# Kernel tuning notes

Measured on AMD Instinct MI355X. Metric: run time of the kernel, lower is better.

## Reference

```python
import jax, jax.numpy as jnp
import numpy as np

EPS = 1e-7
N = 100000
E = 1600000
IN_DIM = 128
OUT_DIM = 128


def _norm(t):
    # clamped L2 norm over last dim, keepdims
    return jnp.clip(jnp.linalg.norm(t, axis=-1, keepdims=True), EPS, None)


def log_map_zero(x, c):
    sqrt_c = jnp.sqrt(c)
    xn = _norm(x)
    y = jnp.clip(sqrt_c * xn, None, 1.0 - 1e-5)
    return jnp.arctanh(y) * x / (sqrt_c * xn)


def exp_map_zero(v, c):
    sqrt_c = jnp.sqrt(c)
    vn = _norm(v)
    return jnp.tanh(sqrt_c * vn) * v / (sqrt_c * vn)


def setup_inputs() -> dict:
    key = jax.random.key(0)
    k1, k2, k3, k4 = jax.random.split(key, 4)
    x = 0.1 * jax.random.normal(k1, (N, IN_DIM), dtype=jnp.float32)  # inside ball
    edge_index = jax.random.randint(k2, (2, E), 0, N, dtype=jnp.int64)
    c = jnp.ones((), dtype=jnp.float32)
    # Xavier-uniform weight (out_dim, in_dim)
    limit = float(np.sqrt(6.0 / (IN_DIM + OUT_DIM)))
    weight = jax.random.uniform(k3, (OUT_DIM, IN_DIM), minval=-limit, maxval=limit, dtype=jnp.float32)
    bias = jnp.zeros((OUT_DIM,), dtype=jnp.float32)
    return {"x": x, "edge_index": edge_index, "c": c, "num_nodes": N,
            "weight": weight, "bias": bias}


def reference(x, edge_index, c, num_nodes, weight, bias):
    # 1. log-map all node features to tangent space at origin
    v = log_map_zero(x, c)  # (N, in_dim)
    src, dst = edge_index[0], edge_index[1]
    # 2. mean aggregation over neighbours (incl. self) via segment_sum
    agg = jax.ops.segment_sum(v[src], dst, num_segments=num_nodes) + v
    count = jax.ops.segment_sum(jnp.ones((src.shape[0],), dtype=v.dtype), dst,
                                num_segments=num_nodes) + 1.0
    v_agg = agg / jnp.clip(count, 1.0, None)[:, None]
    # 3. back to hyperbolic space, then hyperbolic linear
    x_hyp = exp_map_zero(v_agg, c)
    v2 = log_map_zero(x_hyp, c)
    out = v2 @ weight.T + bias
    return exp_map_zero(out, c)
```

## Files before the change

### kernel.cpp

```cpp
#include <hip/hip_runtime.h>
#include <math.h>

#define EPSF 1e-7f
#define YMAXF 0.99999f
#define WPITCH 136

#define NBUCK 256
#define PB_CHUNK 2048

typedef short bf16x8 __attribute__((ext_vector_type(8)));
typedef short bf16x4 __attribute__((ext_vector_type(4)));
typedef float f32x4  __attribute__((ext_vector_type(4)));
typedef int   i32x4  __attribute__((ext_vector_type(4)));

__device__ __forceinline__ float grp32_sum(float v) {
    v += __shfl_xor(v, 1);
    v += __shfl_xor(v, 2);
    v += __shfl_xor(v, 4);
    v += __shfl_xor(v, 8);
    v += __shfl_xor(v, 16);
    return v;
}

__device__ __forceinline__ short f2bf(float f) {
    unsigned u = __float_as_uint(f);
    unsigned r = (u + 0x7FFFu + ((u >> 16) & 1u)) >> 16;
    return (short)r;
}

__device__ __forceinline__ float bf2f(short u) {
    return __uint_as_float(((unsigned)(unsigned short)u) << 16);
}

__device__ __forceinline__ float bf_lo(int w) {
    return __uint_as_float(((unsigned)w) << 16);
}
__device__ __forceinline__ float bf_hi(int w) {
    return __uint_as_float(((unsigned)w) & 0xffff0000u);
}

__global__ void logmap_kernel(const float* __restrict__ x,
                              const float* __restrict__ c_ptr,
                              short* __restrict__ v_bf,
                              int N) {
    int gid = blockIdx.x * blockDim.x + threadIdx.x;
    int row = gid >> 5;
    if (row >= N) return;
    int lane = gid & 31;
    const float4 xv = ((const float4*)x)[(size_t)row * 32 + lane];
    float ss = xv.x * xv.x + xv.y * xv.y + xv.z * xv.z + xv.w * xv.w;
    ss = grp32_sum(ss);
    float sc = sqrtf(c_ptr[0]);
    float xn = fmaxf(sqrtf(ss), EPSF);
    float y = fminf(sc * xn, YMAXF);
    float s = atanhf(y) / (sc * xn);
    bf16x4 pk;
    pk[0] = f2bf(s * xv.x); pk[1] = f2bf(s * xv.y);
    pk[2] = f2bf(s * xv.z); pk[3] = f2bf(s * xv.w);
    *(bf16x4*)&v_bf[(size_t)row * 128 + lane * 4] = pk;
}

__global__ __launch_bounds__(256)
void bucket_count_kernel(const int* __restrict__ eidx_dst,
                         int* __restrict__ bucketCount, int E) {
    __shared__ int h[NBUCK];
    int tid = threadIdx.x;
    h[tid] = 0;
    __syncthreads();
    int per = (E + gridDim.x - 1) / gridDim.x;
    int start = blockIdx.x * per;
    int end = min(start + per, E);
    for (int i = start + tid; i < end; i += 256)
        atomicAdd(&h[eidx_dst[i] >> 9], 1);
    __syncthreads();
    if (h[tid]) atomicAdd(&bucketCount[tid], h[tid]);
}

__global__ __launch_bounds__(256)
void bucket_scan_kernel(const int* __restrict__ bucketCount,
                        int* __restrict__ bucket_base,
                        int* __restrict__ cursor) {
    __shared__ int part[256];
    int tid = threadIdx.x;
    int val = bucketCount[tid];
    part[tid] = val;
    __syncthreads();
    for (int off = 1; off < 256; off <<= 1) {
        int t = (tid >= off) ? part[tid - off] : 0;
        __syncthreads();
        part[tid] += t;
        __syncthreads();
    }
    int excl = part[tid] - val;
    bucket_base[tid] = excl;
    cursor[tid] = excl;
}

__global__ __launch_bounds__(256)
void bucket_scatter_kernel(const int* __restrict__ eidx,
                           int* __restrict__ cursor,
                           int* __restrict__ bucketed, int E) {
    __shared__ int hist[NBUCK];
    __shared__ int lstart[NBUCK];
    __shared__ int gbase[NBUCK];
    __shared__ int part[256];
    __shared__ int stage[PB_CHUNK];
    __shared__ unsigned char stageB[PB_CHUNK];

    int tid = threadIdx.x;
    int start = blockIdx.x * PB_CHUNK;
    int cnt = min(PB_CHUNK, E - start);
    hist[tid] = 0;
    __syncthreads();

    const int J = PB_CHUNK / 256;
    int myP[J], myB[J], myR[J];
    #pragma unroll
    for (int j = 0; j < J; ++j) {
        int idx = j * 256 + tid;
        myR[j] = -1;
        if (idx < cnt) {
            int e = start + idx;
            int d = eidx[E + e];
            int s = eidx[e];
            int b = d >> 9;
            myB[j] = b;
            myP[j] = ((d & 511) << 17) | s;
            myR[j] = atomicAdd(&hist[b], 1);
        }
    }
    __syncthreads();
    part[tid] = hist[tid];
    __syncthreads();
    for (int off = 1; off < 256; off <<= 1) {
        int t = (tid >= off) ? part[tid - off] : 0;
        __syncthreads();
        part[tid] += t;
        __syncthreads();
    }
    lstart[tid] = part[tid] - hist[tid];
    if (hist[tid]) gbase[tid] = atomicAdd(&cursor[tid], hist[tid]);
    __syncthreads();
    #pragma unroll
    for (int j = 0; j < J; ++j) {
        if (myR[j] >= 0) {
            int pos = lstart[myB[j]] + myR[j];
            stage[pos] = myP[j];
            stageB[pos] = (unsigned char)myB[j];
        }
    }
    __syncthreads();
    for (int i = tid; i < cnt; i += 256) {
        int b = stageB[i];
        bucketed[gbase[b] + (i - lstart[b])] = stage[i];
    }
}

__global__ __launch_bounds__(256)
void csr_kernel(const int* __restrict__ bucketed,
                const int* __restrict__ bucket_base,
                const int* __restrict__ cursor_post,
                int* __restrict__ offsets, int* __restrict__ deg,
                int* __restrict__ sorted_src, int N) {
    __shared__ int hist[512];
    __shared__ int pre[512];
    __shared__ int cur[512];
    __shared__ int part[256];
    int b = blockIdx.x;
    int tid = threadIdx.x;
    int start = bucket_base[b];
    int end = cursor_post[b];
    hist[tid] = 0;
    hist[tid + 256] = 0;
    __syncthreads();
    for (int i = start + tid; i < end; i += 256)
        atomicAdd(&hist[bucketed[i] >> 17], 1);
    __syncthreads();
    int a0 = hist[2 * tid], a1 = hist[2 * tid + 1];
    part[tid] = a0 + a1;
    __syncthreads();
    for (int off = 1; off < 256; off <<= 1) {
        int t = (tid >= off) ? part[tid - off] : 0;
        __syncthreads();
        part[tid] += t;
        __syncthreads();
    }
    int base2 = part[tid] - (a0 + a1);
    pre[2 * tid] = base2;
    pre[2 * tid + 1] = base2 + a0;
    cur[2 * tid] = base2;
    cur[2 * tid + 1] = base2 + a0;
    __syncthreads();
    int node0 = b << 9;
    for (int i = tid; i < 512; i += 256) {
        int node = node0 + i;
        if (node < N) { offsets[node] = start + pre[i]; deg[node] = hist[i]; }
    }
    for (int i = start + tid; i < end; i += 256) {
        int p = bucketed[i];
        int ld = p >> 17;
        int src = p & 0x1FFFF;
        int r = atomicAdd(&cur[ld], 1);
        sorted_src[start + r] = src;
    }
}

__global__ __launch_bounds__(256, 3)
void gather_epilogue_kernel(const short* __restrict__ v_bf,
                            const int* __restrict__ sorted_src,
                            const int* __restrict__ offsets,
                            const int* __restrict__ deg,
                            const float* __restrict__ W,
                            const float* __restrict__ bias,
                            const float* __restrict__ c_ptr,
                            float* __restrict__ out,
                            int N) {
    __shared__ short Wl[128 * WPITCH];
    __shared__ short v2l[64 * WPITCH];

    int tid = threadIdx.x;
    for (int i = tid; i < 4096; i += 256) {
        float4 w4 = ((const float4*)W)[i];
        int o = i >> 5;
        int k = (i & 31) * 4;
        bf16x4 w;
        w[0] = f2bf(w4.x); w[1] = f2bf(w4.y); w[2] = f2bf(w4.z); w[3] = f2bf(w4.w);
        *(bf16x4*)&Wl[o * WPITCH + k] = w;
    }

    int wave = tid >> 6;
    int lane = tid & 63;
    int quad = lane >> 4;
    int l16  = lane & 15;
    int g  = tid >> 4;
    int gl = tid & 15;
    float sc = sqrtf(c_ptr[0]);

    float bsv[8];
    #pragma unroll
    for (int c = 0; c < 8; ++c) bsv[c] = bias[c * 16 + l16];

    int row_base = blockIdx.x * 64;

    for (int t = 0; t < 4; ++t) {
        int row = row_base + t * 16 + g;
        bool valid = (row < N);
        float acc[8];
        #pragma unroll
        for (int i = 0; i < 8; ++i) acc[i] = 0.0f;
        int start = 0, d = 0;
        if (valid) {
            start = offsets[row];
            d = deg[row];
            bf16x8 r0 = *(const bf16x8*)&v_bf[(size_t)row * 128 + gl * 8];
            i32x4 w0 = *(const i32x4*)&r0;
            #pragma unroll
            for (int k2 = 0; k2 < 4; ++k2) {
                acc[2 * k2]     = bf_lo(w0[k2]);
                acc[2 * k2 + 1] = bf_hi(w0[k2]);
            }
        }
        for (int j = 0; j < d; j += 16) {
            int m = d - j;
            int batch = sorted_src[start + min(j + gl, d - 1)];

            bf16x8 q0, q1, q2, q3, q4, q5, q6, q7,
                   q8, q9, qA, qB, qC, qD, qE, qF;
#define GLD(i, dst) do {                                                      \
        int src_ = __shfl(batch, (lane & 48) | (i));                          \
        unsigned voff_ = ((unsigned)src_ << 8) | (unsigned)(gl << 4);         \
        asm volatile("global_load_dwordx4 %0, %1, %2"                         \
                     : "=v"(dst) : "v"(voff_), "s"(v_bf));                    \
    } while (0)
            GLD(0, q0);  GLD(1, q1);  GLD(2, q2);  GLD(3, q3);
            GLD(4, q4);  GLD(5, q5);  GLD(6, q6);  GLD(7, q7);
            GLD(8, q8);  GLD(9, q9);  GLD(10, qA); GLD(11, qB);
            GLD(12, qC); GLD(13, qD); GLD(14, qE); GLD(15, qF);
#undef GLD
            asm volatile("s_waitcnt vmcnt(0)" ::: "memory");
            __builtin_amdgcn_sched_barrier(0);

#define ACC(i, rsrc) do {                                                     \
        float w_ = ((i) < m) ? 1.0f : 0.0f;                                   \
        i32x4 wv_ = *(i32x4*)&(rsrc);                                         \
        acc[0] = fmaf(bf_lo(wv_[0]), w_, acc[0]);                             \
        acc[1] = fmaf(bf_hi(wv_[0]), w_, acc[1]);                             \
        acc[2] = fmaf(bf_lo(wv_[1]), w_, acc[2]);                             \
        acc[3] = fmaf(bf_hi(wv_[1]), w_, acc[3]);                             \
        acc[4] = fmaf(bf_lo(wv_[2]), w_, acc[4]);                             \
        acc[5] = fmaf(bf_hi(wv_[2]), w_, acc[5]);                             \
        acc[6] = fmaf(bf_lo(wv_[3]), w_, acc[6]);                             \
        acc[7] = fmaf(bf_hi(wv_[3]), w_, acc[7]);                             \
    } while (0)
            ACC(0, q0);  ACC(1, q1);  ACC(2, q2);  ACC(3, q3);
            ACC(4, q4);  ACC(5, q5);  ACC(6, q6);  ACC(7, q7);
            ACC(8, q8);  ACC(9, q9);  ACC(10, qA); ACC(11, qB);
            ACC(12, qC); ACC(13, qD); ACC(14, qE); ACC(15, qF);
#undef ACC
        }
        float inv = 1.0f / (float)(d + 1);
        #pragma unroll
        for (int i = 0; i < 8; ++i) acc[i] *= inv;

        float ss = 0.0f;
        #pragma unroll
        for (int i = 0; i < 8; ++i) ss += acc[i] * acc[i];
        ss += __shfl_xor(ss, 1);
        ss += __shfl_xor(ss, 2);
        ss += __shfl_xor(ss, 4);
        ss += __shfl_xor(ss, 8);

        float vn  = sqrtf(ss);
        float vnc = fmaxf(vn, EPSF);
        float th  = tanhf(sc * vnc);
        float tt  = th / (sc * vnc);
        float hn  = fmaxf(th / sc, EPSF);
        float y2  = fminf(sc * hn, YMAXF);
        float s2  = atanhf(y2) / (sc * hn);
        float scale = s2 * tt;

        bf16x8 pk;
        #pragma unroll
        for (int i = 0; i < 8; ++i) pk[i] = f2bf(acc[i] * scale);
        *(bf16x8*)&v2l[(t * 16 + g) * WPITCH + gl * 8] = pk;
    }
    __syncthreads();

    f32x4 acc2[8];
    #pragma unroll
    for (int c = 0; c < 8; ++c) acc2[c] = (f32x4){bsv[c], bsv[c], bsv[c], bsv[c]};
    #pragma unroll
    for (int k0 = 0; k0 < 128; k0 += 32) {
        bf16x8 af = *(const bf16x8*)&v2l[(wave * 16 + l16) * WPITCH + k0 + quad * 8];
        #pragma unroll
        for (int c = 0; c < 8; ++c) {
            bf16x8 bf = *(const bf16x8*)&Wl[(c * 16 + l16) * WPITCH + k0 + quad * 8];
            acc2[c] = __builtin_amdgcn_mfma_f32_16x16x32_bf16(af, bf, acc2[c], 0, 0, 0);
        }
    }

    #pragma unroll
    for (int r = 0; r < 4; ++r) {
        float ss = 0.0f;
        #pragma unroll
        for (int c = 0; c < 8; ++c) ss += acc2[c][r] * acc2[c][r];
        ss += __shfl_xor(ss, 1);
        ss += __shfl_xor(ss, 2);
        ss += __shfl_xor(ss, 4);
        ss += __shfl_xor(ss, 8);
        float on  = sqrtf(ss);
        float onc = fmaxf(on, EPSF);
        float gsc = tanhf(sc * onc) / (sc * onc);
        int orow = row_base + wave * 16 + quad * 4 + r;
        if (orow < N) {
            size_t base = (size_t)orow * 128;
            #pragma unroll
            for (int c = 0; c < 8; ++c)
                out[base + c * 16 + l16] = gsc * acc2[c][r];
        }
    }
}

extern "C" void kernel_launch(void* const* d_in, const int* in_sizes, int n_in,
                              void* d_out, int out_size, void* d_ws, size_t ws_size,
                              hipStream_t stream) {
    const float* x     = (const float*)d_in[0];
    const int*   eidx  = (const int*)d_in[1];
    const float* c_ptr = (const float*)d_in[2];
    const float* W     = (const float*)d_in[4];
    const float* bias  = (const float*)d_in[5];
    float* out = (float*)d_out;

    int N = in_sizes[0] / 128;
    int E = in_sizes[1] / 2;

    short* v_bf        = (short*)d_ws;
    int*   deg         = (int*)(v_bf + (size_t)N * 128);
    int*   offsets     = deg + N;
    int*   bucketCount = offsets + N;
    int*   bucket_base = bucketCount + NBUCK;
    int*   cursor      = bucket_base + NBUCK;
    int*   bucketed    = cursor + NBUCK;
    int*   sorted_src  = bucketed + E;

    hipMemsetAsync(bucketCount, 0, NBUCK * sizeof(int), stream);

    {
        long long threads = (long long)N * 32;
        int blocks = (int)((threads + 255) / 256);
        hipLaunchKernelGGL(logmap_kernel, dim3(blocks), dim3(256), 0, stream,
                           x, c_ptr, v_bf, N);
    }
    hipLaunchKernelGGL(bucket_count_kernel, dim3(256), dim3(256), 0, stream,
                       eidx + E, bucketCount, E);
    hipLaunchKernelGGL(bucket_scan_kernel, dim3(1), dim3(256), 0, stream,
                       bucketCount, bucket_base, cursor);
    {
        int blocks = (E + PB_CHUNK - 1) / PB_CHUNK;
        hipLaunchKernelGGL(bucket_scatter_kernel, dim3(blocks), dim3(256), 0, stream,
                           eidx, cursor, bucketed, E);
    }
    {
        int blocks = (N + 511) / 512;
        hipLaunchKernelGGL(csr_kernel, dim3(blocks), dim3(256), 0, stream,
                           bucketed, bucket_base, cursor, offsets, deg, sorted_src, N);
    }
    {
        int blocks = (N + 63) / 64;
        hipLaunchKernelGGL(gather_epilogue_kernel, dim3(blocks), dim3(256), 0, stream,
                           v_bf, sorted_src, offsets, deg, W, bias, c_ptr, out, N);
    }
}
```

Baseline: 266.8 us.

## Replace bucketed CSR build with global atomic counting sort and prep fusion

```diff
diff --git a/kernel.cpp b/kernel.cpp
--- a/kernel.cpp
+++ b/kernel.cpp
@@ -4,9 +4,7 @@
 #define EPSF 1e-7f
 #define YMAXF 0.99999f
 #define WPITCH 136
-
-#define NBUCK 256
-#define PB_CHUNK 2048
+#define SCN 2048
 
 typedef short bf16x8 __attribute__((ext_vector_type(8)));
 typedef short bf16x4 __attribute__((ext_vector_type(4)));
@@ -28,10 +26,6 @@
     return (short)r;
 }
 
-__device__ __forceinline__ float bf2f(short u) {
-    return __uint_as_float(((unsigned)(unsigned short)u) << 16);
-}
-
 __device__ __forceinline__ float bf_lo(int w) {
     return __uint_as_float(((unsigned)w) << 16);
 }
@@ -39,51 +33,72 @@
     return __uint_as_float(((unsigned)w) & 0xffff0000u);
 }
 
-__global__ void logmap_kernel(const float* __restrict__ x,
-                              const float* __restrict__ c_ptr,
-                              short* __restrict__ v_bf,
-                              int N) {
+__global__ __launch_bounds__(256)
+void prep_kernel(const float* __restrict__ x,
+                 const float* __restrict__ c_ptr,
+                 short* __restrict__ v_bf,
+                 const float* __restrict__ W,
+                 short* __restrict__ W_bf,
+                 const int* __restrict__ eidx,
+                 int* __restrict__ deg,
+                 int N, int E) {
     int gid = blockIdx.x * blockDim.x + threadIdx.x;
     int row = gid >> 5;
-    if (row >= N) return;
-    int lane = gid & 31;
-    const float4 xv = ((const float4*)x)[(size_t)row * 32 + lane];
-    float ss = xv.x * xv.x + xv.y * xv.y + xv.z * xv.z + xv.w * xv.w;
-    ss = grp32_sum(ss);
-    float sc = sqrtf(c_ptr[0]);
-    float xn = fmaxf(sqrtf(ss), EPSF);
-    float y = fminf(sc * xn, YMAXF);
-    float s = atanhf(y) / (sc * xn);
-    bf16x4 pk;
-    pk[0] = f2bf(s * xv.x); pk[1] = f2bf(s * xv.y);
-    pk[2] = f2bf(s * xv.z); pk[3] = f2bf(s * xv.w);
-    *(bf16x4*)&v_bf[(size_t)row * 128 + lane * 4] = pk;
+    if (row < N) {
+        int lane = gid & 31;
+        const float4 xv = ((const float4*)x)[(size_t)row * 32 + lane];
+        float ss = xv.x * xv.x + xv.y * xv.y + xv.z * xv.z + xv.w * xv.w;
+        ss = grp32_sum(ss);
+        float sc = sqrtf(c_ptr[0]);
+        float xn = fmaxf(sqrtf(ss), EPSF);
+        float y = fminf(sc * xn, YMAXF);
+        float s = atanhf(y) / (sc * xn);
+        bf16x4 pk;
+        pk[0] = f2bf(s * xv.x); pk[1] = f2bf(s * xv.y);
+        pk[2] = f2bf(s * xv.z); pk[3] = f2bf(s * xv.w);
+        *(bf16x4*)&v_bf[(size_t)row * 128 + lane * 4] = pk;
+    }
+    if (gid < 4096) {
+        float4 w4 = ((const float4*)W)[gid];
+        bf16x4 w;
+        w[0] = f2bf(w4.x); w[1] = f2bf(w4.y); w[2] = f2bf(w4.z); w[3] = f2bf(w4.w);
+        *(bf16x4*)&W_bf[gid * 4] = w;
+    }
+    if (gid < E) {
+        atomicAdd(&deg[eidx[E + gid]], 1);
+    }
 }
 
 __global__ __launch_bounds__(256)
-void bucket_count_kernel(const int* __restrict__ eidx_dst,
-                         int* __restrict__ bucketCount, int E) {
-    __shared__ int h[NBUCK];
-    int tid = threadIdx.x;
-    h[tid] = 0;
+void scan_kernel(const int* __restrict__ deg,
+                 int* __restrict__ offsets,
+                 int* __restrict__ cursor, int N) {
+    __shared__ int part[256];
+    __shared__ int base_s;
+    int blk = blockIdx.x, tid = threadIdx.x;
+    int lim = blk * SCN;
+
+    int bsum = 0;
+    for (int i = tid; i < lim; i += 256) bsum += deg[i];
+    part[tid] = bsum;
     __syncthreads();
-    int per = (E + gridDim.x - 1) / gridDim.x;
-    int start = blockIdx.x * per;
-    int end = min(start + per, E);
-    for (int i = start + tid; i < end; i += 256)
-        atomicAdd(&h[eidx_dst[i] >> 9], 1);
+    for (int off = 128; off; off >>= 1) {
+        if (tid < off) part[tid] += part[tid + off];
+        __syncthreads();
+    }
+    if (tid == 0) base_s = part[0];
     __syncthreads();
-    if (h[tid]) atomicAdd(&bucketCount[tid], h[tid]);
-}
-
-__global__ __launch_bounds__(256)
-void bucket_scan_kernel(const int* __restrict__ bucketCount,
-                        int* __restrict__ bucket_base,
-                        int* __restrict__ cursor) {
-    __shared__ int part[256];
-    int tid = threadIdx.x;
-    int val = bucketCount[tid];
-    part[tid] = val;
+
+    int v[8];
+    int idx0 = lim + tid * 8;
+    int tsum = 0;
+    #pragma unroll
+    for (int j = 0; j < 8; ++j) {
+        int id = idx0 + j;
+        v[j] = (id < N) ? deg[id] : 0;
+        tsum += v[j];
+    }
+    part[tid] = tsum;
     __syncthreads();
     for (int off = 1; off < 256; off <<= 1) {
         int t = (tid >= off) ? part[tid - off] : 0;
@@ -91,143 +106,40 @@
         part[tid] += t;
         __syncthreads();
     }
-    int excl = part[tid] - val;
-    bucket_base[tid] = excl;
-    cursor[tid] = excl;
+    int run = base_s + part[tid] - tsum;
+    #pragma unroll
+    for (int j = 0; j < 8; ++j) {
+        int id = idx0 + j;
+        if (id < N) { offsets[id] = run; cursor[id] = run; }
+        run += v[j];
+    }
 }
 
 __global__ __launch_bounds__(256)
-void bucket_scatter_kernel(const int* __restrict__ eidx,
-                           int* __restrict__ cursor,
-                           int* __restrict__ bucketed, int E) {
-    __shared__ int hist[NBUCK];
-    __shared__ int lstart[NBUCK];
-    __shared__ int gbase[NBUCK];
-    __shared__ int part[256];
-    __shared__ int stage[PB_CHUNK];
-    __shared__ unsigned char stageB[PB_CHUNK];
-
-    int tid = threadIdx.x;
-    int start = blockIdx.x * PB_CHUNK;
-    int cnt = min(PB_CHUNK, E - start);
-    hist[tid] = 0;
-    __syncthreads();
-
-    const int J = PB_CHUNK / 256;
-    int myP[J], myB[J], myR[J];
-    #pragma unroll
-    for (int j = 0; j < J; ++j) {
-        int idx = j * 256 + tid;
-        myR[j] = -1;
-        if (idx < cnt) {
-            int e = start + idx;
-            int d = eidx[E + e];
-            int s = eidx[e];
-            int b = d >> 9;
-            myB[j] = b;
-            myP[j] = ((d & 511) << 17) | s;
-            myR[j] = atomicAdd(&hist[b], 1);
-        }
-    }
-    __syncthreads();
-    part[tid] = hist[tid];
-    __syncthreads();
-    for (int off = 1; off < 256; off <<= 1) {
-        int t = (tid >= off) ? part[tid - off] : 0;
-        __syncthreads();
-        part[tid] += t;
-        __syncthreads();
-    }
-    lstart[tid] = part[tid] - hist[tid];
-    if (hist[tid]) gbase[tid] = atomicAdd(&cursor[tid], hist[tid]);
-    __syncthreads();
-    #pragma unroll
-    for (int j = 0; j < J; ++j) {
-        if (myR[j] >= 0) {
-            int pos = lstart[myB[j]] + myR[j];
-            stage[pos] = myP[j];
-            stageB[pos] = (unsigned char)myB[j];
-        }
-    }
-    __syncthreads();
-    for (int i = tid; i < cnt; i += 256) {
-        int b = stageB[i];
-        bucketed[gbase[b] + (i - lstart[b])] = stage[i];
-    }
-}
-
-__global__ __launch_bounds__(256)
-void csr_kernel(const int* __restrict__ bucketed,
-                const int* __restrict__ bucket_base,
-                const int* __restrict__ cursor_post,
-                int* __restrict__ offsets, int* __restrict__ deg,
-                int* __restrict__ sorted_src, int N) {
-    __shared__ int hist[512];
-    __shared__ int pre[512];
-    __shared__ int cur[512];
-    __shared__ int part[256];
-    int b = blockIdx.x;
-    int tid = threadIdx.x;
-    int start = bucket_base[b];
-    int end = cursor_post[b];
-    hist[tid] = 0;
-    hist[tid + 256] = 0;
-    __syncthreads();
-    for (int i = start + tid; i < end; i += 256)
-        atomicAdd(&hist[bucketed[i] >> 17], 1);
-    __syncthreads();
-    int a0 = hist[2 * tid], a1 = hist[2 * tid + 1];
-    part[tid] = a0 + a1;
-    __syncthreads();
-    for (int off = 1; off < 256; off <<= 1) {
-        int t = (tid >= off) ? part[tid - off] : 0;
-        __syncthreads();
-        part[tid] += t;
-        __syncthreads();
-    }
-    int base2 = part[tid] - (a0 + a1);
-    pre[2 * tid] = base2;
-    pre[2 * tid + 1] = base2 + a0;
-    cur[2 * tid] = base2;
-    cur[2 * tid + 1] = base2 + a0;
-    __syncthreads();
-    int node0 = b << 9;
-    for (int i = tid; i < 512; i += 256) {
-        int node = node0 + i;
-        if (node < N) { offsets[node] = start + pre[i]; deg[node] = hist[i]; }
-    }
-    for (int i = start + tid; i < end; i += 256) {
-        int p = bucketed[i];
-        int ld = p >> 17;
-        int src = p & 0x1FFFF;
-        int r = atomicAdd(&cur[ld], 1);
-        sorted_src[start + r] = src;
-    }
-}
-
-__global__ __launch_bounds__(256, 3)
+void scatter_kernel(const int* __restrict__ eidx,
+                    int* __restrict__ cursor,
+                    int* __restrict__ sorted_src, int E) {
+    int e = blockIdx.x * 256 + threadIdx.x;
+    if (e >= E) return;
+    int s = eidx[e];
+    int d = eidx[E + e];
+    int pos = atomicAdd(&cursor[d], 1);
+    sorted_src[pos] = s;
+}
+
+__global__ __launch_bounds__(256, 4)
 void gather_epilogue_kernel(const short* __restrict__ v_bf,
                             const int* __restrict__ sorted_src,
                             const int* __restrict__ offsets,
                             const int* __restrict__ deg,
-                            const float* __restrict__ W,
+                            const short* __restrict__ W_bf,
                             const float* __restrict__ bias,
                             const float* __restrict__ c_ptr,
                             float* __restrict__ out,
                             int N) {
-    __shared__ short Wl[128 * WPITCH];
     __shared__ short v2l[64 * WPITCH];
 
     int tid = threadIdx.x;
-    for (int i = tid; i < 4096; i += 256) {
-        float4 w4 = ((const float4*)W)[i];
-        int o = i >> 5;
-        int k = (i & 31) * 4;
-        bf16x4 w;
-        w[0] = f2bf(w4.x); w[1] = f2bf(w4.y); w[2] = f2bf(w4.z); w[3] = f2bf(w4.w);
-        *(bf16x4*)&Wl[o * WPITCH + k] = w;
-    }
-
     int wave = tid >> 6;
     int lane = tid & 63;
     int quad = lane >> 4;
@@ -266,6 +178,7 @@
 
             bf16x8 q0, q1, q2, q3, q4, q5, q6, q7,
                    q8, q9, qA, qB, qC, qD, qE, qF;
+            __builtin_amdgcn_sched_barrier(0);
 #define GLD(i, dst) do {                                                      \
         int src_ = __shfl(batch, (lane & 48) | (i));                          \
         unsigned voff_ = ((unsigned)src_ << 8) | (unsigned)(gl << 4);         \
@@ -277,7 +190,7 @@
             GLD(8, q8);  GLD(9, q9);  GLD(10, qA); GLD(11, qB);
             GLD(12, qC); GLD(13, qD); GLD(14, qE); GLD(15, qF);
 #undef GLD
-            asm volatile("s_waitcnt vmcnt(0)" ::: "memory");
+            asm volatile("s_waitcnt vmcnt(8)" ::: "memory");
             __builtin_amdgcn_sched_barrier(0);
 
 #define ACC(i, rsrc) do {                                                     \
@@ -294,6 +207,8 @@
     } while (0)
             ACC(0, q0);  ACC(1, q1);  ACC(2, q2);  ACC(3, q3);
             ACC(4, q4);  ACC(5, q5);  ACC(6, q6);  ACC(7, q7);
+            asm volatile("s_waitcnt vmcnt(0)" ::: "memory");
+            __builtin_amdgcn_sched_barrier(0);
             ACC(8, q8);  ACC(9, q9);  ACC(10, qA); ACC(11, qB);
             ACC(12, qC); ACC(13, qD); ACC(14, qE); ACC(15, qF);
 #undef ACC
@@ -334,8 +249,8 @@
         bf16x8 af = *(const bf16x8*)&v2l[(wave * 16 + l16) * WPITCH + k0 + quad * 8];
         #pragma unroll
         for (int c = 0; c < 8; ++c) {
-            bf16x8 bf = *(const bf16x8*)&Wl[(c * 16 + l16) * WPITCH + k0 + quad * 8];
-            acc2[c] = __builtin_amdgcn_mfma_f32_16x16x32_bf16(af, bf, acc2[c], 0, 0, 0);
+            bf16x8 bw = *(const bf16x8*)&W_bf[(c * 16 + l16) * 128 + k0 + quad * 8];
+            acc2[c] = __builtin_amdgcn_mfma_f32_16x16x32_bf16(af, bw, acc2[c], 0, 0, 0);
         }
     }
 
@@ -377,37 +292,33 @@
     short* v_bf        = (short*)d_ws;
     int*   deg         = (int*)(v_bf + (size_t)N * 128);
     int*   offsets     = deg + N;
-    int*   bucketCount = offsets + N;
-    int*   bucket_base = bucketCount + NBUCK;
-    int*   cursor      = bucket_base + NBUCK;
-    int*   bucketed    = cursor + NBUCK;
-    int*   sorted_src  = bucketed + E;
-
-    hipMemsetAsync(bucketCount, 0, NBUCK * sizeof(int), stream);
+    int*   cursor      = offsets + N;
+    short* W_bf        = (short*)(cursor + N);
+    int*   sorted_src  = (int*)(W_bf + 128 * 128);
+
+    hipMemsetAsync(deg, 0, (size_t)N * sizeof(int), stream);
 
     {
-        long long threads = (long long)N * 32;
+        long long t_log = (long long)N * 32;
+        long long t_cnt = (long long)E;
+        long long threads = t_log > t_cnt ? t_log : t_cnt;
         int blocks = (int)((threads + 255) / 256);
-        hipLaunchKernelGGL(logmap_kernel, dim3(blocks), dim3(256), 0, stream,
-                           x, c_ptr, v_bf, N);
-    }
-    hipLaunchKernelGGL(bucket_count_kernel, dim3(256), dim3(256), 0, stream,
-                       eidx + E, bucketCount, E);
-    hipLaunchKernelGGL(bucket_scan_kernel, dim3(1), dim3(256), 0, stream,
-                       bucketCount, bucket_base, cursor);
+        hipLaunchKernelGGL(prep_kernel, dim3(blocks), dim3(256), 0, stream,
+                           x, c_ptr, v_bf, W, W_bf, eidx, deg, N, E);
+    }
     {
-        int blocks = (E + PB_CHUNK - 1) / PB_CHUNK;
-        hipLaunchKernelGGL(bucket_scatter_kernel, dim3(blocks), dim3(256), 0, stream,
-                           eidx, cursor, bucketed, E);
+        int blocks = (N + SCN - 1) / SCN;
+        hipLaunchKernelGGL(scan_kernel, dim3(blocks), dim3(256), 0, stream,
+                           deg, offsets, cursor, N);
     }
     {
-        int blocks = (N + 511) / 512;
-        hipLaunchKernelGGL(csr_kernel, dim3(blocks), dim3(256), 0, stream,
-                           bucketed, bucket_base, cursor, offsets, deg, sorted_src, N);
+        int blocks = (E + 255) / 256;
+        hipLaunchKernelGGL(scatter_kernel, dim3(blocks), dim3(256), 0, stream,
+                           eidx, cursor, sorted_src, E);
     }
     {
         int blocks = (N + 63) / 64;
         hipLaunchKernelGGL(gather_epilogue_kernel, dim3(blocks), dim3(256), 0, stream,
-                           v_bf, sorted_src, offsets, deg, W, bias, c_ptr, out, N);
-    }
-}
+                           v_bf, sorted_src, offsets, deg, W_bf, bias, c_ptr, out, N);
+    }
+}
```

New measurement: 426.8 us. +60.0%, slower.
